# Kernel optimization log

Hardware: AMD Instinct MI355X
Metric: run time of the kernel (lower is better)

The kernel has to match this reference:

```python
import jax, jax.numpy as jnp
import numpy as np

B, N, D = 8, 2048, 64  # batch, tokens, model dim (heads=1, value_dim=dim)


def _ln(x, g, b, eps=1e-5):
    m = jnp.mean(x, axis=-1, keepdims=True)
    v = jnp.var(x, axis=-1, keepdims=True)
    return (x - m) * jax.lax.rsqrt(v + eps) * g + b


def setup_inputs() -> dict:
    key = jax.random.key(0)
    ks = jax.random.split(key, 6)
    s = lambda k, shp, fan: jax.random.normal(k, shp, jnp.float32) * (fan ** -0.5)
    return {
        "x": jax.random.normal(ks[0], (B, N, D), jnp.float32),
        "Wq": s(ks[1], (D, D), D),            # to_q (no bias)
        "Wkv": s(ks[2], (D, 2 * D), D),       # to_kv -> [k | v] (no bias)
        "ln_mid_g": jnp.ones((D,), jnp.float32),
        "ln_mid_b": jnp.zeros((D,), jnp.float32),
        "rn_in_W": s(ks[3], (3 * D, D), 3 * D),  # RN inner Linear (depth 0)
        "rn_in_b": jnp.zeros((D,), jnp.float32),
        "rn_out_W": s(ks[4], (D, D), D),         # RN outer Linear (depth 0)
        "rn_out_b": jnp.zeros((D,), jnp.float32),
        "ln_out_g": jnp.ones((D,), jnp.float32),
        "ln_out_b": jnp.zeros((D,), jnp.float32),
    }


def reference(x, Wq, Wkv, ln_mid_g, ln_mid_b, rn_in_W, rn_in_b, rn_out_W, rn_out_b, ln_out_g, ln_out_b):
    d = x.shape[-1]
    # --- Relation (heads=1, context = x) ---
    q = x @ Wq                                  # [B,N,D]
    kv = x @ Wkv                                # [B,N,2D]
    k, v = kv[..., :d], kv[..., d:]
    dots = jnp.einsum('bid,bjd->bij', q, k) * (d ** -0.5)   # [B,N,N]
    w = jax.nn.softmax(dots, axis=-1)
    attn = jnp.einsum('bij,bjd->bid', w, v)                  # soft attention
    idx = jnp.argmax(w, axis=-1)                              # [B,N] hard select
    rtn = jnp.take_along_axis(v, idx[..., None], axis=1)      # gather values [B,N,D]
    rtn = attn - jax.lax.stop_gradient(attn - rtn)            # straight-through
    # --- RelationBlock tail (heads=1 => head axis is trivial) ---
    norm = _ln(rtn, ln_mid_g, ln_mid_b)                       # LN_mid per head
    pair = jnp.concatenate([norm, x, norm], axis=-1)          # [relation | residual | relation]
    mid = jax.nn.relu(pair @ rn_in_W + rn_in_b)               # RN inner (depth 0) + ReLU mid
    rn = mid @ rn_out_W + rn_out_b                            # RN outer (depth 0)
    out = _ln(rn, ln_out_g, ln_out_b) + x                     # LN_out + residual
    return out
```

## Files before the change

kernel.cpp:

```cpp
#include <hip/hip_runtime.h>
#include <float.h>

#define NB 8
#define NN 2048
#define ROWS (NB*NN)
#define JSPLIT 8
#define JRANGE (NN/JSPLIT)
#define CHUNK 64
#define NTILE (CHUNK/16)

typedef _Float16 half8 __attribute__((ext_vector_type(8)));
typedef _Float16 half4 __attribute__((ext_vector_type(4)));
typedef float f32x4 __attribute__((ext_vector_type(4)));

__global__ __launch_bounds__(256) void qkv_kernel(
    const float* __restrict__ x, const float* __restrict__ Wq,
    const float* __restrict__ Wkv,
    float* __restrict__ q, float* __restrict__ k, float* __restrict__ v) {
  __shared__ float stage[32*196];
  const int tid = threadIdx.x, lane = tid & 63, wv = tid >> 6;
  const int li = lane & 15, lg = lane >> 4;
  const size_t r0 = (size_t)blockIdx.x * 32;
  half8 xh[2][2], xl[2][2];
#pragma unroll
  for (int rt = 0; rt < 2; ++rt)
#pragma unroll
    for (int kh_ = 0; kh_ < 2; ++kh_) {
      const float* src = x + (r0 + rt*16 + li)*64 + kh_*32 + lg*8;
      float4 f0 = *(const float4*)src;
      float4 f1 = *(const float4*)(src+4);
      float vals[8] = {f0.x,f0.y,f0.z,f0.w,f1.x,f1.y,f1.z,f1.w};
#pragma unroll
      for (int e = 0; e < 8; ++e) {
        _Float16 h = (_Float16)vals[e];
        xh[rt][kh_][e] = h;
        xl[rt][kh_][e] = (_Float16)((vals[e] - (float)h) * 2048.0f);
      }
    }
  half8 wh[3][2], wl[3][2];
#pragma unroll
  for (int ci = 0; ci < 3; ++ci) {
    const int ct = wv*3 + ci;
    const int c  = ct*16 + li;
    const float* base; int strideW;
    if (ct < 4) { base = Wq + c; strideW = 64; }
    else        { base = Wkv + (c - 64); strideW = 128; }
#pragma unroll
    for (int kh_ = 0; kh_ < 2; ++kh_) {
      const int kbase = kh_*32 + lg*8;
#pragma unroll
      for (int e = 0; e < 8; ++e) {
        float val = base[(size_t)(kbase + e) * strideW];
        _Float16 h = (_Float16)val;
        wh[ci][kh_][e] = h;
        wl[ci][kh_][e] = (_Float16)((val - (float)h) * 2048.0f);
      }
    }
  }
  const f32x4 Z = {0.f,0.f,0.f,0.f};
#pragma unroll
  for (int rt = 0; rt < 2; ++rt)
#pragma unroll
    for (int ci = 0; ci < 3; ++ci) {
      f32x4 hh = __builtin_amdgcn_mfma_f32_16x16x32_f16(wh[ci][0], xh[rt][0], Z, 0,0,0);
      hh = __builtin_amdgcn_mfma_f32_16x16x32_f16(wh[ci][1], xh[rt][1], hh, 0,0,0);
      f32x4 xx = __builtin_amdgcn_mfma_f32_16x16x32_f16(wl[ci][0], xh[rt][0], Z, 0,0,0);
      xx = __builtin_amdgcn_mfma_f32_16x16x32_f16(wl[ci][1], xh[rt][1], xx, 0,0,0);
      xx = __builtin_amdgcn_mfma_f32_16x16x32_f16(wh[ci][0], xl[rt][0], xx, 0,0,0);
      xx = __builtin_amdgcn_mfma_f32_16x16x32_f16(wh[ci][1], xl[rt][1], xx, 0,0,0);
      const float c2 = 1.0f/2048.0f;
      float s0 = fmaf(xx[0], c2, hh[0]);
      float s1 = fmaf(xx[1], c2, hh[1]);
      float s2 = fmaf(xx[2], c2, hh[2]);
      float s3 = fmaf(xx[3], c2, hh[3]);
      *(float4*)&stage[(rt*16 + li)*196 + (wv*3+ci)*16 + lg*4] = make_float4(s0,s1,s2,s3);
    }
  __syncthreads();
  const size_t obase = r0 * 64;
#pragma unroll
  for (int it = 0; it < 2; ++it) {
    const int off = it*1024 + tid*4;
    const int row = off >> 6, col = off & 63;
    *(float4*)(q + obase + off) = *(const float4*)&stage[row*196 + col];
    *(float4*)(k + obase + off) = *(const float4*)&stage[row*196 + 64 + col];
    *(float4*)(v + obase + off) = *(const float4*)&stage[row*196 + 128 + col];
  }
}

__global__ __launch_bounds__(256,4) void argmax_mfma_kernel(
    const float* __restrict__ q, const float* __restrict__ k,
    float* __restrict__ pm, int* __restrict__ pt) {
  __shared__ _Float16 kls[2][8][CHUNK][8];
  const int tid = threadIdx.x, lane = tid & 63, wv = tid >> 6;
  const int ib = blockIdx.x, js = blockIdx.y, b = blockIdx.z;
  const int i0 = ib*128 + wv*32;
  const int lg = lane >> 4, li = lane & 15;
  half8 qh[2][2], ql[2][2];
#pragma unroll
  for (int c = 0; c < 2; ++c)
#pragma unroll
    for (int w = 0; w < 2; ++w) {
      const float* src = q + ((size_t)(b*NN + i0 + c*16 + li))*64 + w*32 + lg*8;
      float4 f0 = *(const float4*)src;
      float4 f1 = *(const float4*)(src+4);
      float vals[8] = {f0.x,f0.y,f0.z,f0.w,f1.x,f1.y,f1.z,f1.w};
#pragma unroll
      for (int e = 0; e < 8; ++e) {
        _Float16 h = (_Float16)vals[e];
        qh[c][w][e] = h;
        ql[c][w][e] = (_Float16)((vals[e] - (float)h) * 2048.0f);
      }
    }
  const f32x4 Z = {0.f,0.f,0.f,0.f};
  float mrun[2] = {-FLT_MAX, -FLT_MAX};
  int   trun[2] = {0, 0};
  const int j0base = js*JRANGE;
#pragma unroll 1
  for (int ch = 0; ch < JRANGE/CHUNK; ++ch) {
    const int j0 = j0base + ch*CHUNK;
    __syncthreads();
#pragma unroll
    for (int it = 0; it < 4; ++it) {
      int c = it*256 + tid;
      int j = c & 63, dq = c >> 6;
      const float4 f = *(const float4*)(k + ((size_t)(b*NN + j0 + j))*64 + dq*4);
      float vv[4] = {f.x,f.y,f.z,f.w};
      half4 h, l;
#pragma unroll
      for (int e = 0; e < 4; ++e) {
        _Float16 hh = (_Float16)vv[e];
        h[e] = hh;
        l[e] = (_Float16)((vv[e] - (float)hh) * 2048.0f);
      }
      int d0 = dq >> 1, eo = (dq & 1)*4;
      *(half4*)&kls[0][d0][j][eo] = h;
      *(half4*)&kls[1][d0][j][eo] = l;
    }
    __syncthreads();
#pragma unroll
    for (int jt = 0; jt < NTILE; ++jt) {
      half8 akh0 = *(const half8*)&kls[0][lg  ][jt*16+li][0];
      half8 akh1 = *(const half8*)&kls[0][4+lg][jt*16+li][0];
      half8 akl0 = *(const half8*)&kls[1][lg  ][jt*16+li][0];
      half8 akl1 = *(const half8*)&kls[1][4+lg][jt*16+li][0];
      const int gtile = j0/16 + jt;
#pragma unroll
      for (int c = 0; c < 2; ++c) {
        f32x4 hh = __builtin_amdgcn_mfma_f32_16x16x32_f16(akh0, qh[c][0], Z, 0,0,0);
        hh = __builtin_amdgcn_mfma_f32_16x16x32_f16(akh1, qh[c][1], hh, 0,0,0);
        f32x4 xx = __builtin_amdgcn_mfma_f32_16x16x32_f16(akl0, qh[c][0], Z, 0,0,0);
        xx = __builtin_amdgcn_mfma_f32_16x16x32_f16(akl1, qh[c][1], xx, 0,0,0);
        xx = __builtin_amdgcn_mfma_f32_16x16x32_f16(akh0, ql[c][0], xx, 0,0,0);
        xx = __builtin_amdgcn_mfma_f32_16x16x32_f16(akh1, ql[c][1], xx, 0,0,0);
        const float c2 = 1.0f/2048.0f;
        float s0 = fmaf(xx[0], c2, hh[0]);
        float s1 = fmaf(xx[1], c2, hh[1]);
        float s2 = fmaf(xx[2], c2, hh[2]);
        float s3 = fmaf(xx[3], c2, hh[3]);
        float tmax = fmaxf(fmaxf(s0,s1), fmaxf(s2,s3));
        if (tmax > mrun[c]) { mrun[c] = tmax; trun[c] = gtile; }
      }
    }
  }
#pragma unroll
  for (int c = 0; c < 2; ++c) {
#pragma unroll
    for (int mask = 16; mask <= 32; mask <<= 1) {
      float om = __shfl_xor(mrun[c], mask, 64);
      int   ot = __shfl_xor(trun[c], mask, 64);
      if (om > mrun[c] || (om == mrun[c] && ot < trun[c])) { mrun[c]=om; trun[c]=ot; }
    }
  }
  if (lane < 16) {
    size_t r = (size_t)js*ROWS + b*NN + i0 + lane;
    pm[r] = mrun[0]; pt[r] = trun[0];
  } else if (lane < 32) {
    size_t r = (size_t)js*ROWS + b*NN + i0 + 16 + (lane & 15);
    pm[r] = mrun[1]; pt[r] = trun[1];
  }
}

__global__ __launch_bounds__(256) void epilogue_kernel(
    const float* __restrict__ x, const float* __restrict__ v,
    const float* __restrict__ q, const float* __restrict__ k,
    const float* __restrict__ pm, const int* __restrict__ pt,
    const float* __restrict__ g1, const float* __restrict__ b1,
    const float* __restrict__ W1, const float* __restrict__ bin,
    const float* __restrict__ W2, const float* __restrict__ bout,
    const float* __restrict__ g2, const float* __restrict__ b2,
    float* __restrict__ out) {
  __shared__ float mids[16*68];
  __shared__ float2 sums[16*4];
  __shared__ int sidx[32];
  const int tid = threadIdx.x, lane = tid & 63, wv = tid >> 6;
  const int li = lane & 15, lg = lane >> 4;
  const size_t r0 = (size_t)blockIdx.x * 32;

#pragma unroll
  for (int rnd = 0; rnd < 2; ++rnd) {
    const int rloc = rnd*16 + wv*4 + lg;
    const int row  = (int)r0 + rloc;
    const int b    = row >> 11;
    float m = -FLT_MAX; int t = 0x7fffffff;
    if (li < 8) { m = pm[(size_t)li*ROWS + row]; t = pt[(size_t)li*ROWS + row]; }
#pragma unroll
    for (int mask = 1; mask <= 8; mask <<= 1) {
      float om = __shfl_xor(m, mask, 64);
      int   ot = __shfl_xor(t, mask, 64);
      if (om > m || (om == m && ot < t)) { m = om; t = ot; }
    }
    const int j = t*16 + li;
    const float4* qp = (const float4*)(q + (size_t)row*64);
    const float4* kp = (const float4*)(k + ((size_t)(b*NN) + j)*64);
    float a0=0.f,a1=0.f,a2=0.f,a3=0.f;
#pragma unroll
    for (int d4 = 0; d4 < 16; ++d4) {
      float4 qv = qp[d4], kv = kp[d4];
      a0 = fmaf(qv.x,kv.x,a0); a1 = fmaf(qv.y,kv.y,a1);
      a2 = fmaf(qv.z,kv.z,a2); a3 = fmaf(qv.w,kv.w,a3);
    }
    float dot = (a0+a1)+(a2+a3);
    int bj = j;
#pragma unroll
    for (int mask = 1; mask <= 8; mask <<= 1) {
      float od = __shfl_xor(dot, mask, 64);
      int   oj = __shfl_xor(bj, mask, 64);
      if (od > dot || (od == dot && oj < bj)) { dot = od; bj = oj; }
    }
    if (li == 0) sidx[rloc] = bj;
  }

  half8 wah[2], wal[2], wbh[2], wbl[2], w2h[2], w2l[2];
  const int ocol = wv*16 + li;
#pragma unroll
  for (int kh_ = 0; kh_ < 2; ++kh_) {
#pragma unroll
    for (int e = 0; e < 8; ++e) {
      const int d = kh_*32 + lg*8 + e;
      float wa = W1[d*64 + ocol] + W1[(128+d)*64 + ocol];
      float wb = W1[(64+d)*64 + ocol];
      float w2 = W2[d*64 + ocol];
      _Float16 h;
      h = (_Float16)wa; wah[kh_][e]=h; wal[kh_][e]=(_Float16)((wa-(float)h)*2048.f);
      h = (_Float16)wb; wbh[kh_][e]=h; wbl[kh_][e]=(_Float16)((wb-(float)h)*2048.f);
      h = (_Float16)w2; w2h[kh_][e]=h; w2l[kh_][e]=(_Float16)((w2-(float)h)*2048.f);
    }
  }
  float ga[16], bb[16];
  *(float4*)&ga[0]  = *(const float4*)(g1 + lg*8);
  *(float4*)&ga[4]  = *(const float4*)(g1 + lg*8 + 4);
  *(float4*)&ga[8]  = *(const float4*)(g1 + 32 + lg*8);
  *(float4*)&ga[12] = *(const float4*)(g1 + 32 + lg*8 + 4);
  *(float4*)&bb[0]  = *(const float4*)(b1 + lg*8);
  *(float4*)&bb[4]  = *(const float4*)(b1 + lg*8 + 4);
  *(float4*)&bb[8]  = *(const float4*)(b1 + 32 + lg*8);
  *(float4*)&bb[12] = *(const float4*)(b1 + 32 + lg*8 + 4);
  const float4 binv  = *(const float4*)(bin + wv*16 + lg*4);
  const float4 boutv = *(const float4*)(bout + wv*16 + lg*4);
  const float4 g2v   = *(const float4*)(g2 + wv*16 + lg*4);
  const float4 b2v   = *(const float4*)(b2 + wv*16 + lg*4);
  __syncthreads();

  const f32x4 Z = {0.f,0.f,0.f,0.f};
  const float c2 = 1.0f/2048.0f;
#pragma unroll 1
  for (int p = 0; p < 2; ++p) {
    const int rr = (int)r0 + p*16 + li;
    const int b  = rr >> 11;
    const int j  = sidx[p*16 + li];
    const float* vsrc = v + ((size_t)b*NN + j)*64 + lg*8;
    const float* xsrc = x + (size_t)rr*64 + lg*8;
    float vv[16], xv[16];
    *(float4*)&vv[0]  = *(const float4*)(vsrc);
    *(float4*)&vv[4]  = *(const float4*)(vsrc+4);
    *(float4*)&vv[8]  = *(const float4*)(vsrc+32);
    *(float4*)&vv[12] = *(const float4*)(vsrc+36);
    *(float4*)&xv[0]  = *(const float4*)(xsrc);
    *(float4*)&xv[4]  = *(const float4*)(xsrc+4);
    *(float4*)&xv[8]  = *(const float4*)(xsrc+32);
    *(float4*)&xv[12] = *(const float4*)(xsrc+36);
    float s = 0.f, s2 = 0.f;
#pragma unroll
    for (int e = 0; e < 16; ++e) { s += vv[e]; s2 += vv[e]*vv[e]; }
#pragma unroll
    for (int mask = 16; mask <= 32; mask <<= 1) {
      s  += __shfl_xor(s,  mask, 64);
      s2 += __shfl_xor(s2, mask, 64);
    }
    float mu  = s*(1.f/64.f);
    float inv = rsqrtf(s2*(1.f/64.f) - mu*mu + 1e-5f);
    half8 nh[2], nl[2], xh[2], xl[2];
#pragma unroll
    for (int kh_ = 0; kh_ < 2; ++kh_)
#pragma unroll
      for (int e = 0; e < 8; ++e) {
        float nvv = (vv[kh_*8+e] - mu)*inv*ga[kh_*8+e] + bb[kh_*8+e];
        _Float16 h = (_Float16)nvv;
        nh[kh_][e] = h; nl[kh_][e] = (_Float16)((nvv - (float)h)*2048.f);
        float xvv = xv[kh_*8+e];
        h = (_Float16)xvv;
        xh[kh_][e] = h; xl[kh_][e] = (_Float16)((xvv - (float)h)*2048.f);
      }
    f32x4 hh = __builtin_amdgcn_mfma_f32_16x16x32_f16(wah[0], nh[0], Z, 0,0,0);
    hh = __builtin_amdgcn_mfma_f32_16x16x32_f16(wah[1], nh[1], hh, 0,0,0);
    hh = __builtin_amdgcn_mfma_f32_16x16x32_f16(wbh[0], xh[0], hh, 0,0,0);
    hh = __builtin_amdgcn_mfma_f32_16x16x32_f16(wbh[1], xh[1], hh, 0,0,0);
    f32x4 xx = __builtin_amdgcn_mfma_f32_16x16x32_f16(wal[0], nh[0], Z, 0,0,0);
    xx = __builtin_amdgcn_mfma_f32_16x16x32_f16(wal[1], nh[1], xx, 0,0,0);
    xx = __builtin_amdgcn_mfma_f32_16x16x32_f16(wah[0], nl[0], xx, 0,0,0);
    xx = __builtin_amdgcn_mfma_f32_16x16x32_f16(wah[1], nl[1], xx, 0,0,0);
    xx = __builtin_amdgcn_mfma_f32_16x16x32_f16(wbl[0], xh[0], xx, 0,0,0);
    xx = __builtin_amdgcn_mfma_f32_16x16x32_f16(wbl[1], xh[1], xx, 0,0,0);
    xx = __builtin_amdgcn_mfma_f32_16x16x32_f16(wbh[0], xl[0], xx, 0,0,0);
    xx = __builtin_amdgcn_mfma_f32_16x16x32_f16(wbh[1], xl[1], xx, 0,0,0);
    float mv0 = fmaxf(fmaf(xx[0], c2, hh[0]) + binv.x, 0.f);
    float mv1 = fmaxf(fmaf(xx[1], c2, hh[1]) + binv.y, 0.f);
    float mv2 = fmaxf(fmaf(xx[2], c2, hh[2]) + binv.z, 0.f);
    float mv3 = fmaxf(fmaf(xx[3], c2, hh[3]) + binv.w, 0.f);
    *(float4*)&mids[li*68 + wv*16 + lg*4] = make_float4(mv0,mv1,mv2,mv3);
    __syncthreads();
    half8 mh[2], ml[2];
#pragma unroll
    for (int kh_ = 0; kh_ < 2; ++kh_) {
      float mm[8];
      *(float4*)&mm[0] = *(const float4*)&mids[li*68 + kh_*32 + lg*8];
      *(float4*)&mm[4] = *(const float4*)&mids[li*68 + kh_*32 + lg*8 + 4];
#pragma unroll
      for (int e = 0; e < 8; ++e) {
        _Float16 h = (_Float16)mm[e];
        mh[kh_][e] = h; ml[kh_][e] = (_Float16)((mm[e] - (float)h)*2048.f);
      }
    }
    __syncthreads();
    f32x4 h2 = __builtin_amdgcn_mfma_f32_16x16x32_f16(w2h[0], mh[0], Z, 0,0,0);
    h2 = __builtin_amdgcn_mfma_f32_16x16x32_f16(w2h[1], mh[1], h2, 0,0,0);
    f32x4 x2 = __builtin_amdgcn_mfma_f32_16x16x32_f16(w2l[0], mh[0], Z, 0,0,0);
    x2 = __builtin_amdgcn_mfma_f32_16x16x32_f16(w2l[1], mh[1], x2, 0,0,0);
    x2 = __builtin_amdgcn_mfma_f32_16x16x32_f16(w2h[0], ml[0], x2, 0,0,0);
    x2 = __builtin_amdgcn_mfma_f32_16x16x32_f16(w2h[1], ml[1], x2, 0,0,0);
    float rn[4];
    rn[0] = fmaf(x2[0], c2, h2[0]) + boutv.x;
    rn[1] = fmaf(x2[1], c2, h2[1]) + boutv.y;
    rn[2] = fmaf(x2[2], c2, h2[2]) + boutv.z;
    rn[3] = fmaf(x2[3], c2, h2[3]) + boutv.w;
    float ps = rn[0]+rn[1]+rn[2]+rn[3];
    float ps2 = rn[0]*rn[0]+rn[1]*rn[1]+rn[2]*rn[2]+rn[3]*rn[3];
#pragma unroll
    for (int mask = 16; mask <= 32; mask <<= 1) {
      ps  += __shfl_xor(ps,  mask, 64);
      ps2 += __shfl_xor(ps2, mask, 64);
    }
    if (lg == 0) sums[li*4 + wv] = make_float2(ps, ps2);
    __syncthreads();
    float ts = 0.f, ts2 = 0.f;
#pragma unroll
    for (int w = 0; w < 4; ++w) { float2 pp = sums[li*4 + w]; ts += pp.x; ts2 += pp.y; }
    float mu2  = ts*(1.f/64.f);
    float inv2 = rsqrtf(ts2*(1.f/64.f) - mu2*mu2 + 1e-5f);
    float4 xnv = *(const float4*)(x + (size_t)rr*64 + wv*16 + lg*4);
    float4 ov;
    ov.x = (rn[0]-mu2)*inv2*g2v.x + b2v.x + xnv.x;
    ov.y = (rn[1]-mu2)*inv2*g2v.y + b2v.y + xnv.y;
    ov.z = (rn[2]-mu2)*inv2*g2v.z + b2v.z + xnv.z;
    ov.w = (rn[3]-mu2)*inv2*g2v.w + b2v.w + xnv.w;
    *(float4*)&mids[li*68 + wv*16 + lg*4] = ov;
    __syncthreads();
    const int row = tid >> 4, col = (tid & 15)*4;
    *(float4*)(out + (r0 + p*16)*64 + tid*4) = *(const float4*)&mids[row*68 + col];
    __syncthreads();
  }
}

extern "C" void kernel_launch(void* const* d_in, const int* in_sizes, int n_in,
                              void* d_out, int out_size, void* d_ws, size_t ws_size,
                              hipStream_t stream) {
  const float* x    = (const float*)d_in[0];
  const float* Wq   = (const float*)d_in[1];
  const float* Wkv  = (const float*)d_in[2];
  const float* g1   = (const float*)d_in[3];
  const float* b1   = (const float*)d_in[4];
  const float* W1   = (const float*)d_in[5];
  const float* bin  = (const float*)d_in[6];
  const float* W2   = (const float*)d_in[7];
  const float* bout = (const float*)d_in[8];
  const float* g2   = (const float*)d_in[9];
  const float* b2   = (const float*)d_in[10];
  float* ws   = (float*)d_ws;
  float* q    = ws;
  float* k    = ws + 1048576;
  float* v    = ws + 2097152;
  float* pm   = ws + 3145728;
  int*   pt   = (int*)(ws + 3276800);

  qkv_kernel<<<ROWS/32, 256, 0, stream>>>(x, Wq, Wkv, q, k, v);
  argmax_mfma_kernel<<<dim3(16, JSPLIT, NB), 256, 0, stream>>>(q, k, pm, pt);
  epilogue_kernel<<<ROWS/32, 256, 0, stream>>>(x, v, q, k, pm, pt, g1, b1, W1, bin,
                                               W2, bout, g2, b2, (float*)d_out);
}
```

Before: 58.47 us.

## Double-buffer K tiles in argmax kernel and batch epilogue passes to cut barriers

The argmax kernel now prefetches the next K chunk into registers while MFMAs run on the current shared-memory buffer, using two LDS buffers and one barrier per chunk instead of two. The epilogue processes both 16-row passes together with larger shared arrays, so the number of __syncthreads drops from about ten to four. Both changes aim to hide global load latency and reduce synchronization stalls. In exchange they raise register and LDS use, which may lower occupancy under launch_bounds(256,4).

After: 61.19 us. +4.6%, slower.

```diff
diff --git a/kernel.cpp b/kernel.cpp
--- a/kernel.cpp
+++ b/kernel.cpp
@@ -8,6 +8,7 @@
 #define JRANGE (NN/JSPLIT)
 #define CHUNK 64
 #define NTILE (CHUNK/16)
+#define NCHUNK (JRANGE/CHUNK)
 
 typedef _Float16 half8 __attribute__((ext_vector_type(8)));
 typedef _Float16 half4 __attribute__((ext_vector_type(4)));
@@ -87,10 +88,29 @@
   }
 }
 
+#define WRITEBUF(BUF)                                                     \
+  {                                                                       \
+    _Pragma("unroll")                                                     \
+    for (int it = 0; it < 4; ++it) {                                      \
+      const int dq = dq0 + it*4;                                          \
+      float vv4[4] = {fst[it].x, fst[it].y, fst[it].z, fst[it].w};        \
+      half4 h, l;                                                         \
+      _Pragma("unroll")                                                   \
+      for (int e = 0; e < 4; ++e) {                                       \
+        _Float16 hh_ = (_Float16)vv4[e];                                  \
+        h[e] = hh_;                                                       \
+        l[e] = (_Float16)((vv4[e] - (float)hh_) * 2048.0f);               \
+      }                                                                   \
+      const int d0 = dq >> 1, eo = (dq & 1)*4;                            \
+      *(half4*)&kls[BUF][0][d0][sj][eo] = h;                              \
+      *(half4*)&kls[BUF][1][d0][sj][eo] = l;                              \
+    }                                                                     \
+  }
+
 __global__ __launch_bounds__(256,4) void argmax_mfma_kernel(
     const float* __restrict__ q, const float* __restrict__ k,
     float* __restrict__ pm, int* __restrict__ pt) {
-  __shared__ _Float16 kls[2][8][CHUNK][8];
+  __shared__ _Float16 kls[2][2][8][CHUNK][8];
   const int tid = threadIdx.x, lane = tid & 63, wv = tid >> 6;
   const int ib = blockIdx.x, js = blockIdx.y, b = blockIdx.z;
   const int i0 = ib*128 + wv*32;
@@ -115,34 +135,30 @@
   float mrun[2] = {-FLT_MAX, -FLT_MAX};
   int   trun[2] = {0, 0};
   const int j0base = js*JRANGE;
+  const int sj = tid & 63;
+  const int dq0 = tid >> 6;
+  float4 fst[4];
+#pragma unroll
+  for (int it = 0; it < 4; ++it)
+    fst[it] = *(const float4*)(k + ((size_t)(b*NN + j0base + sj))*64 + (dq0 + it*4)*4);
+  WRITEBUF(0);
 #pragma unroll 1
-  for (int ch = 0; ch < JRANGE/CHUNK; ++ch) {
+  for (int ch = 0; ch < NCHUNK; ++ch) {
+    __syncthreads();
+    if (ch + 1 < NCHUNK) {
+      const int j0n = j0base + (ch+1)*CHUNK;
+#pragma unroll
+      for (int it = 0; it < 4; ++it)
+        fst[it] = *(const float4*)(k + ((size_t)(b*NN + j0n + sj))*64 + (dq0 + it*4)*4);
+    }
+    const int buf = ch & 1;
     const int j0 = j0base + ch*CHUNK;
-    __syncthreads();
-#pragma unroll
-    for (int it = 0; it < 4; ++it) {
-      int c = it*256 + tid;
-      int j = c & 63, dq = c >> 6;
-      const float4 f = *(const float4*)(k + ((size_t)(b*NN + j0 + j))*64 + dq*4);
-      float vv[4] = {f.x,f.y,f.z,f.w};
-      half4 h, l;
-#pragma unroll
-      for (int e = 0; e < 4; ++e) {
-        _Float16 hh = (_Float16)vv[e];
-        h[e] = hh;
-        l[e] = (_Float16)((vv[e] - (float)hh) * 2048.0f);
-      }
-      int d0 = dq >> 1, eo = (dq & 1)*4;
-      *(half4*)&kls[0][d0][j][eo] = h;
-      *(half4*)&kls[1][d0][j][eo] = l;
-    }
-    __syncthreads();
 #pragma unroll
     for (int jt = 0; jt < NTILE; ++jt) {
-      half8 akh0 = *(const half8*)&kls[0][lg  ][jt*16+li][0];
-      half8 akh1 = *(const half8*)&kls[0][4+lg][jt*16+li][0];
-      half8 akl0 = *(const half8*)&kls[1][lg  ][jt*16+li][0];
-      half8 akl1 = *(const half8*)&kls[1][4+lg][jt*16+li][0];
+      half8 akh0 = *(const half8*)&kls[buf][0][lg  ][jt*16+li][0];
+      half8 akh1 = *(const half8*)&kls[buf][0][4+lg][jt*16+li][0];
+      half8 akl0 = *(const half8*)&kls[buf][1][lg  ][jt*16+li][0];
+      half8 akl1 = *(const half8*)&kls[buf][1][4+lg][jt*16+li][0];
       const int gtile = j0/16 + jt;
 #pragma unroll
       for (int c = 0; c < 2; ++c) {
@@ -161,6 +177,7 @@
         if (tmax > mrun[c]) { mrun[c] = tmax; trun[c] = gtile; }
       }
     }
+    if (ch + 1 < NCHUNK) WRITEBUF((ch+1)&1);
   }
 #pragma unroll
   for (int c = 0; c < 2; ++c) {
@@ -189,8 +206,8 @@
     const float* __restrict__ W2, const float* __restrict__ bout,
     const float* __restrict__ g2, const float* __restrict__ b2,
     float* __restrict__ out) {
-  __shared__ float mids[16*68];
-  __shared__ float2 sums[16*4];
+  __shared__ float mids[32*68];
+  __shared__ float2 sums[32*4];
   __shared__ int sidx[32];
   const int tid = threadIdx.x, lane = tid & 63, wv = tid >> 6;
   const int li = lane & 15, lg = lane >> 4;
@@ -263,7 +280,8 @@
 
   const f32x4 Z = {0.f,0.f,0.f,0.f};
   const float c2 = 1.0f/2048.0f;
-#pragma unroll 1
+  half8 nh[2][2], nl[2][2], xfh[2][2], xfl[2][2];
+#pragma unroll
   for (int p = 0; p < 2; ++p) {
     const int rr = (int)r0 + p*16 + li;
     const int b  = rr >> 11;
@@ -289,85 +307,99 @@
     }
     float mu  = s*(1.f/64.f);
     float inv = rsqrtf(s2*(1.f/64.f) - mu*mu + 1e-5f);
-    half8 nh[2], nl[2], xh[2], xl[2];
 #pragma unroll
     for (int kh_ = 0; kh_ < 2; ++kh_)
 #pragma unroll
       for (int e = 0; e < 8; ++e) {
         float nvv = (vv[kh_*8+e] - mu)*inv*ga[kh_*8+e] + bb[kh_*8+e];
         _Float16 h = (_Float16)nvv;
-        nh[kh_][e] = h; nl[kh_][e] = (_Float16)((nvv - (float)h)*2048.f);
+        nh[p][kh_][e] = h; nl[p][kh_][e] = (_Float16)((nvv - (float)h)*2048.f);
         float xvv = xv[kh_*8+e];
         h = (_Float16)xvv;
-        xh[kh_][e] = h; xl[kh_][e] = (_Float16)((xvv - (float)h)*2048.f);
-      }
-    f32x4 hh = __builtin_amdgcn_mfma_f32_16x16x32_f16(wah[0], nh[0], Z, 0,0,0);
-    hh = __builtin_amdgcn_mfma_f32_16x16x32_f16(wah[1], nh[1], hh, 0,0,0);
-    hh = __builtin_amdgcn_mfma_f32_16x16x32_f16(wbh[0], xh[0], hh, 0,0,0);
-    hh = __builtin_amdgcn_mfma_f32_16x16x32_f16(wbh[1], xh[1], hh, 0,0,0);
-    f32x4 xx = __builtin_amdgcn_mfma_f32_16x16x32_f16(wal[0], nh[0], Z, 0,0,0);
-    xx = __builtin_amdgcn_mfma_f32_16x16x32_f16(wal[1], nh[1], xx, 0,0,0);
-    xx = __builtin_amdgcn_mfma_f32_16x16x32_f16(wah[0], nl[0], xx, 0,0,0);
-    xx = __builtin_amdgcn_mfma_f32_16x16x32_f16(wah[1], nl[1], xx, 0,0,0);
-    xx = __builtin_amdgcn_mfma_f32_16x16x32_f16(wbl[0], xh[0], xx, 0,0,0);
-    xx = __builtin_amdgcn_mfma_f32_16x16x32_f16(wbl[1], xh[1], xx, 0,0,0);
-    xx = __builtin_amdgcn_mfma_f32_16x16x32_f16(wbh[0], xl[0], xx, 0,0,0);
-    xx = __builtin_amdgcn_mfma_f32_16x16x32_f16(wbh[1], xl[1], xx, 0,0,0);
+        xfh[p][kh_][e] = h; xfl[p][kh_][e] = (_Float16)((xvv - (float)h)*2048.f);
+      }
+  }
+#pragma unroll
+  for (int p = 0; p < 2; ++p) {
+    f32x4 hh = __builtin_amdgcn_mfma_f32_16x16x32_f16(wah[0], nh[p][0], Z, 0,0,0);
+    hh = __builtin_amdgcn_mfma_f32_16x16x32_f16(wah[1], nh[p][1], hh, 0,0,0);
+    hh = __builtin_amdgcn_mfma_f32_16x16x32_f16(wbh[0], xfh[p][0], hh, 0,0,0);
+    hh = __builtin_amdgcn_mfma_f32_16x16x32_f16(wbh[1], xfh[p][1], hh, 0,0,0);
+    f32x4 xx = __builtin_amdgcn_mfma_f32_16x16x32_f16(wal[0], nh[p][0], Z, 0,0,0);
+    xx = __builtin_amdgcn_mfma_f32_16x16x32_f16(wal[1], nh[p][1], xx, 0,0,0);
+    xx = __builtin_amdgcn_mfma_f32_16x16x32_f16(wah[0], nl[p][0], xx, 0,0,0);
+    xx = __builtin_amdgcn_mfma_f32_16x16x32_f16(wah[1], nl[p][1], xx, 0,0,0);
+    xx = __builtin_amdgcn_mfma_f32_16x16x32_f16(wbl[0], xfh[p][0], xx, 0,0,0);
+    xx = __builtin_amdgcn_mfma_f32_16x16x32_f16(wbl[1], xfh[p][1], xx, 0,0,0);
+    xx = __builtin_amdgcn_mfma_f32_16x16x32_f16(wbh[0], xfl[p][0], xx, 0,0,0);
+    xx = __builtin_amdgcn_mfma_f32_16x16x32_f16(wbh[1], xfl[p][1], xx, 0,0,0);
     float mv0 = fmaxf(fmaf(xx[0], c2, hh[0]) + binv.x, 0.f);
     float mv1 = fmaxf(fmaf(xx[1], c2, hh[1]) + binv.y, 0.f);
     float mv2 = fmaxf(fmaf(xx[2], c2, hh[2]) + binv.z, 0.f);
     float mv3 = fmaxf(fmaf(xx[3], c2, hh[3]) + binv.w, 0.f);
-    *(float4*)&mids[li*68 + wv*16 + lg*4] = make_float4(mv0,mv1,mv2,mv3);
-    __syncthreads();
-    half8 mh[2], ml[2];
+    *(float4*)&mids[(p*16+li)*68 + wv*16 + lg*4] = make_float4(mv0,mv1,mv2,mv3);
+  }
+  __syncthreads();
+  half8 mh[2][2], ml[2][2];
+#pragma unroll
+  for (int p = 0; p < 2; ++p)
 #pragma unroll
     for (int kh_ = 0; kh_ < 2; ++kh_) {
       float mm[8];
-      *(float4*)&mm[0] = *(const float4*)&mids[li*68 + kh_*32 + lg*8];
-      *(float4*)&mm[4] = *(const float4*)&mids[li*68 + kh_*32 + lg*8 + 4];
+      *(float4*)&mm[0] = *(const float4*)&mids[(p*16+li)*68 + kh_*32 + lg*8];
+      *(float4*)&mm[4] = *(const float4*)&mids[(p*16+li)*68 + kh_*32 + lg*8 + 4];
 #pragma unroll
       for (int e = 0; e < 8; ++e) {
         _Float16 h = (_Float16)mm[e];
-        mh[kh_][e] = h; ml[kh_][e] = (_Float16)((mm[e] - (float)h)*2048.f);
-      }
-    }
-    __syncthreads();
-    f32x4 h2 = __builtin_amdgcn_mfma_f32_16x16x32_f16(w2h[0], mh[0], Z, 0,0,0);
-    h2 = __builtin_amdgcn_mfma_f32_16x16x32_f16(w2h[1], mh[1], h2, 0,0,0);
-    f32x4 x2 = __builtin_amdgcn_mfma_f32_16x16x32_f16(w2l[0], mh[0], Z, 0,0,0);
-    x2 = __builtin_amdgcn_mfma_f32_16x16x32_f16(w2l[1], mh[1], x2, 0,0,0);
-    x2 = __builtin_amdgcn_mfma_f32_16x16x32_f16(w2h[0], ml[0], x2, 0,0,0);
-    x2 = __builtin_amdgcn_mfma_f32_16x16x32_f16(w2h[1], ml[1], x2, 0,0,0);
-    float rn[4];
-    rn[0] = fmaf(x2[0], c2, h2[0]) + boutv.x;
-    rn[1] = fmaf(x2[1], c2, h2[1]) + boutv.y;
-    rn[2] = fmaf(x2[2], c2, h2[2]) + boutv.z;
-    rn[3] = fmaf(x2[3], c2, h2[3]) + boutv.w;
-    float ps = rn[0]+rn[1]+rn[2]+rn[3];
-    float ps2 = rn[0]*rn[0]+rn[1]*rn[1]+rn[2]*rn[2]+rn[3]*rn[3];
+        mh[p][kh_][e] = h; ml[p][kh_][e] = (_Float16)((mm[e] - (float)h)*2048.f);
+      }
+    }
+  float rnv[2][4];
+#pragma unroll
+  for (int p = 0; p < 2; ++p) {
+    f32x4 h2 = __builtin_amdgcn_mfma_f32_16x16x32_f16(w2h[0], mh[p][0], Z, 0,0,0);
+    h2 = __builtin_amdgcn_mfma_f32_16x16x32_f16(w2h[1], mh[p][1], h2, 0,0,0);
+    f32x4 x2 = __builtin_amdgcn_mfma_f32_16x16x32_f16(w2l[0], mh[p][0], Z, 0,0,0);
+    x2 = __builtin_amdgcn_mfma_f32_16x16x32_f16(w2l[1], mh[p][1], x2, 0,0,0);
+    x2 = __builtin_amdgcn_mfma_f32_16x16x32_f16(w2h[0], ml[p][0], x2, 0,0,0);
+    x2 = __builtin_amdgcn_mfma_f32_16x16x32_f16(w2h[1], ml[p][1], x2, 0,0,0);
+    rnv[p][0] = fmaf(x2[0], c2, h2[0]) + boutv.x;
+    rnv[p][1] = fmaf(x2[1], c2, h2[1]) + boutv.y;
+    rnv[p][2] = fmaf(x2[2], c2, h2[2]) + boutv.z;
+    rnv[p][3] = fmaf(x2[3], c2, h2[3]) + boutv.w;
+    float ps = rnv[p][0]+rnv[p][1]+rnv[p][2]+rnv[p][3];
+    float ps2 = rnv[p][0]*rnv[p][0]+rnv[p][1]*rnv[p][1]
+              + rnv[p][2]*rnv[p][2]+rnv[p][3]*rnv[p][3];
 #pragma unroll
     for (int mask = 16; mask <= 32; mask <<= 1) {
       ps  += __shfl_xor(ps,  mask, 64);
       ps2 += __shfl_xor(ps2, mask, 64);
     }
-    if (lg == 0) sums[li*4 + wv] = make_float2(ps, ps2);
-    __syncthreads();
+    if (lg == 0) sums[(p*16+li)*4 + wv] = make_float2(ps, ps2);
+  }
+  __syncthreads();
+#pragma unroll
+  for (int p = 0; p < 2; ++p) {
     float ts = 0.f, ts2 = 0.f;
 #pragma unroll
-    for (int w = 0; w < 4; ++w) { float2 pp = sums[li*4 + w]; ts += pp.x; ts2 += pp.y; }
+    for (int w = 0; w < 4; ++w) { float2 pp = sums[(p*16+li)*4 + w]; ts += pp.x; ts2 += pp.y; }
     float mu2  = ts*(1.f/64.f);
     float inv2 = rsqrtf(ts2*(1.f/64.f) - mu2*mu2 + 1e-5f);
+    const int rr = (int)r0 + p*16 + li;
     float4 xnv = *(const float4*)(x + (size_t)rr*64 + wv*16 + lg*4);
     float4 ov;
-    ov.x = (rn[0]-mu2)*inv2*g2v.x + b2v.x + xnv.x;
-    ov.y = (rn[1]-mu2)*inv2*g2v.y + b2v.y + xnv.y;
-    ov.z = (rn[2]-mu2)*inv2*g2v.z + b2v.z + xnv.z;
-    ov.w = (rn[3]-mu2)*inv2*g2v.w + b2v.w + xnv.w;
-    *(float4*)&mids[li*68 + wv*16 + lg*4] = ov;
-    __syncthreads();
-    const int row = tid >> 4, col = (tid & 15)*4;
-    *(float4*)(out + (r0 + p*16)*64 + tid*4) = *(const float4*)&mids[row*68 + col];
-    __syncthreads();
+    ov.x = (rnv[p][0]-mu2)*inv2*g2v.x + b2v.x + xnv.x;
+    ov.y = (rnv[p][1]-mu2)*inv2*g2v.y + b2v.y + xnv.y;
+    ov.z = (rnv[p][2]-mu2)*inv2*g2v.z + b2v.z + xnv.z;
+    ov.w = (rnv[p][3]-mu2)*inv2*g2v.w + b2v.w + xnv.w;
+    *(float4*)&mids[(p*16+li)*68 + wv*16 + lg*4] = ov;
+  }
+  __syncthreads();
+#pragma unroll
+  for (int it = 0; it < 2; ++it) {
+    const int off = it*1024 + tid*4;
+    const int row = off >> 6, col = off & 63;
+    *(float4*)(out + r0*64 + off) = *(const float4*)&mids[row*68 + col];
   }
 }
 
```
